# Optimization experiments

Measured on AMD Instinct MI355X. Metric: run time of the kernel, lower is better.

Reference implementation:

```python
import jax, jax.numpy as jnp
import numpy as np

T = 4096          # flattened document length (tokens)
FLAT = 512        # 2 * lstm_hidden_size
HD = 256          # head embedding dim (head_emb + char_emb)
FEAT = 20         # feature_size
MAXW = 20         # max mention width
NCAND = 30000     # enumerated candidate spans
HID = 512         # scorer hidden size
K = 1638          # floor(T * ment_ratio=0.4)
C = 40            # max antecedents
DEPTH = 2         # coref_depth
NSPK = 10
MENT = 2 * FLAT + FEAT + HD        # 1300 mention emb size
BIN_WIDTHS = [1, 1, 1, 1, 1, 4, 8, 16, 32]   # sums to 65 -> covers clamp(dist,0,64)
BINS = jnp.asarray(np.concatenate([np.full(w, i, dtype=np.int32) for i, w in enumerate(BIN_WIDTHS)]))


def _scorer(x, w1, b1, w2, b2, w3, b3):
    h = jax.nn.relu(x @ w1 + b1)
    h = jax.nn.relu(h @ w2 + b2)
    return (h @ w3 + b3)[..., 0]


def setup_inputs():
    key = jax.random.key(0)
    ks = jax.random.split(key, 30)
    p = lambda i, s: jax.random.normal(ks[i], s, jnp.float32) * 0.02
    cand_starts = jax.random.randint(ks[25], (NCAND,), 0, T)
    widths = jax.random.randint(ks[26], (NCAND,), 0, MAXW)
    cand_ends = jnp.minimum(cand_starts + widths, T - 1)
    return {
        "flat_lstm_out": jax.random.normal(ks[0], (T, FLAT), jnp.float32),
        "head_doc_embs": jax.random.normal(ks[1], (T, HD), jnp.float32),
        "w_span_head": p(2, (FLAT,)), "b_span_head": jnp.zeros((), jnp.float32),
        "width_embed": p(3, (MAXW, FEAT)),
        "ms_w1": p(4, (MENT, HID)), "ms_b1": jnp.zeros((HID,), jnp.float32),
        "ms_w2": p(5, (HID, HID)), "ms_b2": jnp.zeros((HID,), jnp.float32),
        "ms_w3": p(6, (HID, 1)), "ms_b3": jnp.zeros((1,), jnp.float32),
        "fast_w": p(7, (MENT, MENT)), "fast_b": jnp.zeros((MENT,), jnp.float32),
        "ss_w1": p(8, (3 * MENT + 3 * FEAT, HID)), "ss_b1": jnp.zeros((HID,), jnp.float32),
        "ss_w2": p(9, (HID, HID)), "ss_b2": jnp.zeros((HID,), jnp.float32),
        "ss_w3": p(10, (HID, 1)), "ss_b3": jnp.zeros((1,), jnp.float32),
        "gate_w": p(11, (2 * MENT, MENT)), "gate_b": jnp.zeros((MENT,), jnp.float32),
        "speaker_embed": p(12, (2, FEAT)),
        "genre_embed": p(13, (7, FEAT)),
        "dist_embed": p(14, (len(BIN_WIDTHS), FEAT)),
        "cand_starts": cand_starts,
        "cand_ends": cand_ends,
        "speaker_ids": jax.random.randint(ks[27], (T,), 0, NSPK),
        "genre_id": 3,
    }


def reference(flat_lstm_out, head_doc_embs, w_span_head, b_span_head, width_embed,
              ms_w1, ms_b1, ms_w2, ms_b2, ms_w3, ms_b3, fast_w, fast_b,
              ss_w1, ss_b1, ss_w2, ss_b2, ss_w3, ss_b3, gate_w, gate_b,
              speaker_embed, genre_embed, dist_embed,
              cand_starts, cand_ends, speaker_ids, genre_id):
    neg = -jnp.inf
    # ---- mention (span) embeddings: start/end gather + width emb + attention-pooled head ----
    width = cand_ends - cand_starts + 1                              # [N]
    start_embs = flat_lstm_out[cand_starts]                          # [N,FLAT]
    end_embs = flat_lstm_out[cand_ends]                              # [N,FLAT]
    width_embs = width_embed[width - 1]                              # [N,FEAT]
    span_idxs = jnp.clip(jnp.arange(MAXW)[None, :] + cand_starts[:, None], 0, T - 1)  # [N,W]
    ment_doc = head_doc_embs[span_idxs]                              # [N,W,HD]
    head_scores = flat_lstm_out @ w_span_head + b_span_head          # [T]
    g = head_scores[span_idxs] + jnp.where(jnp.arange(MAXW)[None, :] < width[:, None], 0.0, neg)
    attn = jax.nn.softmax(g, axis=1)                                 # [N,W]
    head_embs = jnp.einsum('nw,nwd->nd', attn, ment_doc)             # [N,HD]
    cand_embs = jnp.concatenate([start_embs, end_embs, width_embs, head_embs], axis=1)  # [N,MENT]
    cand_scores = _scorer(cand_embs, ms_w1, ms_b1, ms_w2, ms_b2, ms_w3, ms_b3)          # [N]
    # ---- prune mentions: top-k by score, reordered by document position ----
    _, top_idx = jax.lax.top_k(cand_scores, K)
    ment_pos = cand_starts[top_idx] * cand_ends[-1] + cand_ends[top_idx]
    top_idx = top_idx[jnp.argsort(ment_pos)]
    ment_embs = cand_embs[top_idx]                                   # [K,MENT]
    ment_scores = cand_scores[top_idx]                               # [K]
    ment_speakers = speaker_ids[cand_starts[top_idx]]                # [K]
    # ---- fast (bilinear) antecedent scoring + top-c pruning ----
    idx = jnp.arange(K)
    mask = (idx[:, None] - idx[None, :]) > 0                         # antecedent must precede
    src = ment_embs @ fast_w + fast_b
    fast = src @ ment_embs.T + ment_scores[:, None] + ment_scores[None, :] + jnp.where(mask, 0.0, neg)
    top_fast, antes = jax.lax.top_k(fast, C)                         # [K,C]
    dummy = jnp.zeros((K, 1), fast.dtype)
    genre_emb = jnp.broadcast_to(genre_embed[genre_id][None, None, :], (K, C, FEAT))
    ante_scores = top_fast
    # ---- iterative slow antecedent scoring + gated refinement ----
    for _ in range(DEPTH):
        ante_ment = ment_embs[antes]                                 # [K,C,MENT]
        same = (ment_speakers[:, None] == ment_speakers[antes]).astype(jnp.int32)
        spk_emb = speaker_embed[same]                                # [K,C,FEAT]
        dist_bin = BINS[jnp.clip(idx[:, None] - antes, 0, 64)]
        dist_emb = dist_embed[dist_bin]                              # [K,C,FEAT]
        me = jnp.broadcast_to(ment_embs[:, None, :], (K, C, MENT))
        ante_emb = jnp.concatenate([me, ante_ment, ante_ment * me, spk_emb, genre_emb, dist_emb], axis=2)
        ante_scores = top_fast + _scorer(ante_emb, ss_w1, ss_b1, ss_w2, ss_b2, ss_w3, ss_b3)
        weights = jax.nn.softmax(jnp.concatenate([dummy, ante_scores], axis=1), axis=-1)  # [K,C+1]
        stacked = jnp.concatenate([ment_embs[:, None, :], ante_ment], axis=1)             # [K,C+1,MENT]
        attended = jnp.einsum('kc,kcd->kd', weights, stacked)
        f = jax.nn.sigmoid(jnp.concatenate([ment_embs, attended], axis=1) @ gate_w + gate_b)
        ment_embs = f * attended + (1.0 - f) * ment_embs
    return jnp.concatenate([dummy, ante_scores], axis=1)             # [K,C+1] coref logits
```

## Files before the change

### kernel.cpp

```cpp
#include <hip/hip_runtime.h>
#include <math.h>

#define T_LEN 4096
#define FLATD 512
#define HDD 256
#define FEATD 20
#define NCAND 30000
#define HIDD 512
#define KSEL 1638
#define CANT 40
#define MENTD 1300
#define KPAD 1344
#define NPAIR (KSEL*CANT)
#define NEG_INF (-__builtin_inff())

#define MF_RELU 1
#define MF_MASK 4
#define MF_GATE 8

typedef unsigned short u16;
typedef __attribute__((ext_vector_type(8))) short bf16x8;
typedef __attribute__((ext_vector_type(4))) float f32x4;

__device__ __forceinline__ unsigned ordf(float f){
  unsigned u = __float_as_uint(f);
  return (u & 0x80000000u) ? ~u : (u | 0x80000000u);
}
__device__ __forceinline__ float unordf(unsigned u){
  return __uint_as_float((u & 0x80000000u) ? (u ^ 0x80000000u) : ~u);
}
__device__ __forceinline__ float bf2f(u16 h){ return __uint_as_float(((unsigned)h) << 16); }
__device__ __forceinline__ u16 f2bf(float f){
  unsigned u = __float_as_uint(f);
  u += 0x7fffu + ((u >> 16) & 1u);
  return (u16)(u >> 16);
}
__device__ __forceinline__ unsigned pkmul(unsigned a, unsigned b){
  float a0 = __uint_as_float(a << 16), a1 = __uint_as_float(a & 0xffff0000u);
  float b0 = __uint_as_float(b << 16), b1 = __uint_as_float(b & 0xffff0000u);
  float p0 = a0*b0, p1 = a1*b1;
  unsigned r;
  asm("v_cvt_pk_bf16_f32 %0, %1, %2" : "=v"(r) : "v"(p0), "v"(p1));
  return r;
}
__device__ __forceinline__ int featsrc(int k){
  if (k < 1024) return k;
  if (k < 1280) return k + 20;
  if (k < 1300) return k - 256;
  return -1;
}
__device__ __forceinline__ int bsrc64(int S){
  return (((S & 7) ^ ((S >> 3) & 7)) << 3);
}
__device__ __forceinline__ int brd64(int row, int h, int k8){
  return row*64 + (((((h << 2) | k8)) ^ (row & 7)) << 3);
}
__device__ __forceinline__ void gload16(const u16* g, u16* l){
  __builtin_amdgcn_global_load_lds((const __attribute__((address_space(1))) void*)(g),
                                   (__attribute__((address_space(3))) void*)(l), 16, 0, 0);
}

__global__ __launch_bounds__(256) void k_prep(const float* __restrict__ flat,
    const float* __restrict__ wemb, const float* __restrict__ fast_b, const float* __restrict__ gate_b,
    u16* __restrict__ flatbf, u16* __restrict__ wembP, float* __restrict__ fbP, float* __restrict__ gbP,
    unsigned* __restrict__ selws)
{
  int i = blockIdx.x*256 + threadIdx.x;
  if (i < T_LEN*FLATD) flatbf[i] = f2bf(flat[i]);
  if (i < 20*64) wembP[i] = ((i & 63) < 20) ? f2bf(wemb[(i >> 6)*FEATD + (i & 63)]) : (u16)0;
  if (i < KPAD){
    int s = featsrc(i);
    fbP[i] = (s >= 0) ? fast_b[s] : 0.f;
    gbP[i] = (s >= 0) ? gate_b[s] : 0.f;
  }
  if (i < 6156) selws[i] = 0;
}

__global__ __launch_bounds__(256) void k_head(const float* __restrict__ flat,
    const float* __restrict__ w, const float* __restrict__ b, float* __restrict__ hs)
{
  int lane = threadIdx.x & 63, wid = threadIdx.x >> 6;
  int row = blockIdx.x*4 + wid;
  if (row >= T_LEN) return;
  const float* x = flat + (size_t)row*FLATD;
  float s = 0.f;
  for (int j = lane; j < FLATD; j += 64) s += x[j]*w[j];
  #pragma unroll
  for (int o = 32; o; o >>= 1) s += __shfl_down(s, o, 64);
  if (lane == 0) hs[row] = s + b[0];
}

__global__ __launch_bounds__(256) void k_cand(const float* __restrict__ hs,
    const float* __restrict__ hdoc, const int* __restrict__ starts, const int* __restrict__ ends,
    u16* __restrict__ hemb)
{
  int wid = threadIdx.x >> 6, lane = threadIdx.x & 63;
  int n = blockIdx.x*4 + wid;
  if (n >= NCAND) return;
  int s = starts[n], e = ends[n];
  int width = e - s + 1;
  float g[20];
  #pragma unroll
  for (int w2 = 0; w2 < 20; ++w2) g[w2] = (w2 < width) ? hs[min(s + w2, T_LEN-1)] : NEG_INF;
  float m = NEG_INF;
  #pragma unroll
  for (int w2 = 0; w2 < 20; ++w2) m = fmaxf(m, g[w2]);
  float sum = 0.f;
  #pragma unroll
  for (int w2 = 0; w2 < 20; ++w2){ g[w2] = expf(g[w2] - m); sum += g[w2]; }
  float inv = 1.f/sum;
  #pragma unroll
  for (int di = 0; di < 4; ++di){
    int d = lane + di*64;
    float acc = 0.f;
    #pragma unroll
    for (int w2 = 0; w2 < 20; ++w2)
      acc += g[w2]*hdoc[(size_t)min(s + w2, T_LEN-1)*HDD + d];
    hemb[(size_t)n*HDD + d] = f2bf(acc*inv);
  }
}

__global__ __launch_bounds__(256) void k_transall(const float* __restrict__ ms_w1,
    const float* __restrict__ ms_w2, const float* __restrict__ fast_w,
    const float* __restrict__ ss_w1, const float* __restrict__ ss_w2,
    const float* __restrict__ gate_w,
    u16* ms1T, u16* ms2T, u16* fastT, u16* ss1abT, u16* sspT,
    u16* ss2T, u16* gateTall)
{
  const float* B; u16* D; int Kb, N, srcN, ldD, kperm, nperm;
  switch (blockIdx.z){
    case 0: B = ms_w1; D = ms1T; Kb = KPAD; N = HIDD; srcN = HIDD; ldD = KPAD; kperm = 1; nperm = 0; break;
    case 1: B = ms_w2; D = ms2T; Kb = HIDD; N = HIDD; srcN = HIDD; ldD = HIDD; kperm = 0; nperm = 0; break;
    case 2: B = fast_w; D = fastT; Kb = KPAD; N = MENTD; srcN = MENTD; ldD = KPAD; kperm = 1; nperm = 1; break;
    case 3: B = ss_w1; D = ss1abT; Kb = KPAD; N = HIDD; srcN = HIDD; ldD = KPAD; kperm = 1; nperm = 0; break;
    case 4: B = ss_w1 + (size_t)MENTD*HIDD; D = ss1abT + (size_t)512*KPAD; Kb = KPAD; N = HIDD; srcN = HIDD; ldD = KPAD; kperm = 1; nperm = 0; break;
    case 5: B = ss_w1 + (size_t)2*MENTD*HIDD; D = sspT; Kb = KPAD; N = HIDD; srcN = HIDD; ldD = KPAD; kperm = 1; nperm = 0; break;
    case 6: B = ss_w2; D = ss2T; Kb = HIDD; N = HIDD; srcN = HIDD; ldD = HIDD; kperm = 0; nperm = 0; break;
    case 7: B = gate_w; D = gateTall; Kb = KPAD; N = MENTD; srcN = MENTD; ldD = 2*KPAD; kperm = 1; nperm = 1; break;
    default: B = gate_w + (size_t)MENTD*MENTD; D = gateTall + KPAD; Kb = KPAD; N = MENTD; srcN = MENTD; ldD = 2*KPAD; kperm = 1; nperm = 1; break;
  }
  int k0 = blockIdx.x*32, n0 = blockIdx.y*32;
  if (k0 >= Kb || n0 >= N) return;
  __shared__ float t[32][33];
  int tx = threadIdx.x & 31, ty = threadIdx.x >> 5;
  for (int r = ty; r < 32; r += 8){
    int gk = k0 + r, gn = n0 + tx;
    int sk = kperm ? featsrc(gk) : ((gk < Kb) ? gk : -1);
    int sn = nperm ? ((gn < N) ? featsrc(gn) : -1) : ((gn < N) ? gn : -1);
    t[r][tx] = (sk >= 0 && sn >= 0) ? B[(size_t)sk*srcN + sn] : 0.f;
  }
  __syncthreads();
  for (int r = ty; r < 32; r += 8){
    int gn = n0 + r, gk = k0 + tx;
    if (gn < N && gk < Kb) D[(size_t)gn*ldD + gk] = f2bf(t[tx][r]);
  }
}

__global__ __launch_bounds__(256) void k_mfma_cand(
    const u16* __restrict__ flatbf, const u16* __restrict__ hemb, const u16* __restrict__ wembP,
    const int* __restrict__ starts, const int* __restrict__ ends,
    const u16* __restrict__ Bt, int M, const float* __restrict__ bias, u16* __restrict__ Cbf)
{
  __shared__ alignas(16) u16 As[8192];
  __shared__ alignas(16) u16 Bs[8192];
  int tid = threadIdx.x;
  int row0 = blockIdx.y*128, col0 = blockIdx.x*128;
  int lane = tid & 63, wid = tid >> 6;
  int wr = wid >> 1, wc = wid & 1;
  int l15 = lane & 15, l4 = lane >> 4;

  int sS[4], eS[4], nS[4], so[4];
  const u16* pb[4];
  #pragma unroll
  for (int i = 0; i < 4; ++i){
    int S = tid + (i << 8);
    int r = S >> 3;
    so[i] = bsrc64(S);
    int n = row0 + r; if (n >= M) n = M - 1;
    sS[i] = starts[n]; eS[i] = ends[n]; nS[i] = n;
    pb[i] = Bt + (size_t)(col0 + r)*KPAD + so[i];
  }

  f32x4 acc[4][4];
  #pragma unroll
  for (int m = 0; m < 4; ++m)
    #pragma unroll
    for (int n = 0; n < 4; ++n)
      #pragma unroll
      for (int q = 0; q < 4; ++q) acc[m][n][q] = 0.f;

  for (int kt = 0; kt < KPAD/64; ++kt){
    int k0 = kt << 6;
    #pragma unroll
    for (int i = 0; i < 4; ++i){
      int f = k0 + so[i];
      const u16* src = (f < 512) ? flatbf + (size_t)sS[i]*FLATD + f
                     : (f < 1024) ? flatbf + (size_t)eS[i]*FLATD + (f - 512)
                     : (f < 1280) ? hemb + (size_t)nS[i]*HDD + (f - 1024)
                     : wembP + (eS[i] - sS[i])*64 + (f - 1280);
      gload16(src, As + (tid + (i << 8))*8);
      gload16(pb[i] + k0, Bs + (tid + (i << 8))*8);
    }
    __syncthreads();
    #pragma unroll
    for (int h = 0; h < 2; ++h){
      bf16x8 af[4], bfr[4];
      #pragma unroll
      for (int m = 0; m < 4; ++m) af[m] = *(const bf16x8*)(As + brd64(wr*64 + m*16 + l15, h, l4));
      #pragma unroll
      for (int n = 0; n < 4; ++n) bfr[n] = *(const bf16x8*)(Bs + brd64(wc*64 + n*16 + l15, h, l4));
      #pragma unroll
      for (int m = 0; m < 4; ++m)
        #pragma unroll
        for (int n = 0; n < 4; ++n)
          acc[m][n] = __builtin_amdgcn_mfma_f32_16x16x32_bf16(af[m], bfr[n], acc[m][n], 0, 0, 0);
    }
    __syncthreads();
  }
  #pragma unroll
  for (int m = 0; m < 4; ++m){
    #pragma unroll
    for (int q = 0; q < 4; ++q){
      int grow = row0 + wr*64 + m*16 + l4*4 + q;
      if (grow >= M) continue;
      #pragma unroll
      for (int n = 0; n < 4; ++n){
        int gcol = col0 + wc*64 + n*16 + l15;
        float v = fmaxf(acc[m][n][q] + bias[gcol], 0.f);
        Cbf[(size_t)grow*HIDD + gcol] = f2bf(v);
      }
    }
  }
}

__global__ __launch_bounds__(256) void k_mfma(const u16* __restrict__ A,
    const u16* __restrict__ A2, const u16* __restrict__ Bt, int M, int N, int Kp, int ldA,
    const float* __restrict__ bias, const float* __restrict__ msc,
    float* __restrict__ Cf, int ldf, u16* __restrict__ Cbf, int ldbf, int Nstore, int flags,
    const u16* __restrict__ g_att, const u16* __restrict__ g_mo)
{
  __shared__ alignas(16) u16 As[8192];
  __shared__ alignas(16) u16 Bs[8192];
  int tid = threadIdx.x;
  int row0 = blockIdx.y*128, col0 = blockIdx.x*128;
  if ((flags & MF_MASK) && col0 >= row0 + 128) return;
  int lane = tid & 63, wid = tid >> 6;
  int wr = wid >> 1, wc = wid & 1;
  int l15 = lane & 15, l4 = lane >> 4;

  const u16 *pa[4], *qa[4], *pb[4];
  int kt1 = A2 ? (ldA >> 6) : (Kp >> 6);
  int koff = kt1 << 6;
  #pragma unroll
  for (int i = 0; i < 4; ++i){
    int S = tid + (i << 8);
    int r = S >> 3;
    int soi = bsrc64(S);
    int ra = row0 + r; if (ra >= M) ra = M - 1;
    int cb = col0 + r; if (cb >= N) cb = N - 1;
    pa[i] = A + (size_t)ra*ldA + soi;
    qa[i] = A2 ? (A2 + (size_t)ra*ldA + soi - koff) : pa[i];
    pb[i] = Bt + (size_t)cb*Kp + soi;
  }

  f32x4 acc[4][4];
  #pragma unroll
  for (int m = 0; m < 4; ++m)
    #pragma unroll
    for (int n = 0; n < 4; ++n)
      #pragma unroll
      for (int q = 0; q < 4; ++q) acc[m][n][q] = 0.f;

  int nkt = Kp >> 6;
  for (int kt = 0; kt < nkt; ++kt){
    int k0 = kt << 6;
    #pragma unroll
    for (int i = 0; i < 4; ++i){
      const u16* a = (kt < kt1) ? pa[i] : qa[i];
      gload16(a + k0, As + (tid + (i << 8))*8);
      gload16(pb[i] + k0, Bs + (tid + (i << 8))*8);
    }
    __syncthreads();
    #pragma unroll
    for (int h = 0; h < 2; ++h){
      bf16x8 af[4], bfr[4];
      #pragma unroll
      for (int m = 0; m < 4; ++m) af[m] = *(const bf16x8*)(As + brd64(wr*64 + m*16 + l15, h, l4));
      #pragma unroll
      for (int n = 0; n < 4; ++n) bfr[n] = *(const bf16x8*)(Bs + brd64(wc*64 + n*16 + l15, h, l4));
      #pragma unroll
      for (int m = 0; m < 4; ++m)
        #pragma unroll
        for (int n = 0; n < 4; ++n)
          acc[m][n] = __builtin_amdgcn_mfma_f32_16x16x32_bf16(af[m], bfr[n], acc[m][n], 0, 0, 0);
    }
    __syncthreads();
  }
  #pragma unroll
  for (int m = 0; m < 4; ++m){
    #pragma unroll
    for (int q = 0; q < 4; ++q){
      int grow = row0 + wr*64 + m*16 + l4*4 + q;
      if (grow >= M) continue;
      #pragma unroll
      for (int n = 0; n < 4; ++n){
        int gcol = col0 + wc*64 + n*16 + l15;
        if (gcol < N){
          float v = acc[m][n][q];
          if (bias) v += bias[gcol];
          if (flags & MF_MASK){ v += msc[grow] + msc[gcol]; if (gcol >= grow) v = NEG_INF; }
          if (flags & MF_RELU) v = fmaxf(v, 0.f);
          if (flags & MF_GATE){
            float f = 1.f/(1.f + expf(-v));
            float res = f*bf2f(g_att[(size_t)grow*ldbf + gcol])
                      + (1.f - f)*bf2f(g_mo[(size_t)grow*ldbf + gcol]);
            Cbf[(size_t)grow*ldbf + gcol] = f2bf(res);
          } else {
            if (Cf)  Cf[(size_t)grow*ldf + gcol] = v;
            if (Cbf) Cbf[(size_t)grow*ldbf + gcol] = f2bf(v);
          }
        } else if (Cbf && gcol < Nstore){
          Cbf[(size_t)grow*ldbf + gcol] = 0;
        }
      }
    }
  }
}

__global__ __launch_bounds__(256) void k_mfma_rowdot(const u16* __restrict__ A,
    const u16* __restrict__ Bt, int M, const float* __restrict__ b2,
    const float* __restrict__ w3, const float* __restrict__ b3,
    const float* __restrict__ add, float* __restrict__ out)
{
  __shared__ alignas(16) u16 As[8192];
  __shared__ alignas(16) u16 Bs[8192];
  __shared__ float rsum[128][2];
  int tid = threadIdx.x;
  int row0 = blockIdx.x*128;
  int lane = tid & 63, wid = tid >> 6;
  int wr = wid >> 1, wc = wid & 1;
  int l15 = lane & 15, l4 = lane >> 4;

  const u16* pa[4]; int so[4], rr[4];
  #pragma unroll
  for (int i = 0; i < 4; ++i){
    int S = tid + (i << 8);
    int r = S >> 3;
    so[i] = bsrc64(S); rr[i] = r;
    int ra = row0 + r; if (ra >= M) ra = M - 1;
    pa[i] = A + (size_t)ra*HIDD + so[i];
  }

  float rd[4][4] = {};
  for (int p = 0; p < 4; ++p){
    int col0 = p*128;
    f32x4 acc[4][4];
    #pragma unroll
    for (int m = 0; m < 4; ++m)
      #pragma unroll
      for (int n = 0; n < 4; ++n)
        #pragma unroll
        for (int q = 0; q < 4; ++q) acc[m][n][q] = 0.f;
    for (int kt = 0; kt < HIDD/64; ++kt){
      int k0 = kt << 6;
      #pragma unroll
      for (int i = 0; i < 4; ++i){
        gload16(pa[i] + k0, As + (tid + (i << 8))*8);
        gload16(Bt + (size_t)(col0 + rr[i])*HIDD + so[i] + k0, Bs + (tid + (i << 8))*8);
      }
      __syncthreads();
      #pragma unroll
      for (int h = 0; h < 2; ++h){
        bf16x8 af[4], bfr[4];
        #pragma unroll
        for (int m = 0; m < 4; ++m) af[m] = *(const bf16x8*)(As + brd64(wr*64 + m*16 + l15, h, l4));
        #pragma unroll
        for (int n = 0; n < 4; ++n) bfr[n] = *(const bf16x8*)(Bs + brd64(wc*64 + n*16 + l15, h, l4));
        #pragma unroll
        for (int m = 0; m < 4; ++m)
          #pragma unroll
          for (int n = 0; n < 4; ++n)
            acc[m][n] = __builtin_amdgcn_mfma_f32_16x16x32_bf16(af[m], bfr[n], acc[m][n], 0, 0, 0);
      }
      __syncthreads();
    }
    #pragma unroll
    for (int n = 0; n < 4; ++n){
      int gcol = col0 + wc*64 + n*16 + l15;
      float bb = b2[gcol], ww = w3[gcol];
      #pragma unroll
      for (int m = 0; m < 4; ++m)
        #pragma unroll
        for (int q = 0; q < 4; ++q){
          float v = fmaxf(acc[m][n][q] + bb, 0.f);
          rd[m][q] = fmaf(v, ww, rd[m][q]);
        }
    }
  }
  #pragma unroll
  for (int m = 0; m < 4; ++m)
    #pragma unroll
    for (int q = 0; q < 4; ++q){
      float s = rd[m][q];
      s += __shfl_xor(s, 1, 64); s += __shfl_xor(s, 2, 64);
      s += __shfl_xor(s, 4, 64); s += __shfl_xor(s, 8, 64);
      if (l15 == 0) rsum[wr*64 + m*16 + l4*4 + q][wc] = s;
    }
  __syncthreads();
  if (tid < 128){
    int gr = row0 + tid;
    if (gr < M){
      float v = rsum[tid][0] + rsum[tid][1] + b3[0];
      if (add) v += add[gr];
      out[gr] = v;
    }
  }
}

__global__ __launch_bounds__(256, 2) void k_d1_mfma(int Mc,
    const u16* __restrict__ ment, const int* __restrict__ antes, const int* __restrict__ mspk,
    const u16* __restrict__ Bt, const float* __restrict__ A_meb,
    const float* __restrict__ comb, u16* __restrict__ H1)
{
  __shared__ alignas(16) u16 As[8192];
  __shared__ alignas(16) u16 Bs[16384];
  __shared__ int ri[128], rj[128], rcomb[128];
  int tid = threadIdx.x;
  int row0 = blockIdx.y*128;
  int col0 = blockIdx.x*256;
  if (tid < 128){
    int r = row0 + tid;
    int p = (r < Mc ? r : 0);
    int i = p / CANT;
    int j = antes[p];
    ri[tid] = i; rj[tid] = j;
    int same = (mspk[i] == mspk[j]) ? 1 : 0;
    int d = i - j; d = d < 0 ? 0 : (d > 64 ? 64 : d);
    int bin = (d <= 4) ? d : (d <= 8 ? 5 : (d <= 16 ? 6 : (d <= 32 ? 7 : 8)));
    rcomb[tid] = same*9 + bin;
  }
  __syncthreads();
  int lane = tid & 63, wid = tid >> 6;
  int wr = wid >> 1, wc = wid & 1;
  int l15 = lane & 15, l4 = lane >> 4;

  const u16 *pi[4], *pj[4];
  #pragma unroll
  for (int i = 0; i < 4; ++i){
    int S = tid + (i << 8);
    int r = S >> 3;
    int soi = bsrc64(S);
    pi[i] = ment + (size_t)ri[r]*KPAD + soi;
    pj[i] = ment + (size_t)rj[r]*KPAD + soi;
  }
  int bo[8];
  #pragma unroll
  for (int i = 0; i < 8; ++i){
    int S = tid + (i << 8);
    int r = S >> 3;
    bo[i] = (col0 + r)*KPAD + bsrc64(S);
  }

  f32x4 acc[4][8];
  #pragma unroll
  for (int m = 0; m < 4; ++m)
    #pragma unroll
    for (int n = 0; n < 8; ++n)
      #pragma unroll
      for (int q = 0; q < 4; ++q) acc[m][n][q] = 0.f;

  int nkt = KPAD >> 6;
  for (int kt = 0; kt < nkt; ++kt){
    int k0 = kt << 6;
    #pragma unroll
    for (int i = 0; i < 8; ++i)
      gload16(Bt + bo[i] + k0, Bs + (tid + (i << 8))*8);
    #pragma unroll
    for (int i = 0; i < 4; ++i){
      uint4 va = *(const uint4*)(pi[i] + k0);
      uint4 vb = *(const uint4*)(pj[i] + k0);
      uint4 vo;
      vo.x = pkmul(va.x, vb.x); vo.y = pkmul(va.y, vb.y);
      vo.z = pkmul(va.z, vb.z); vo.w = pkmul(va.w, vb.w);
      *(uint4*)(As + (tid + (i << 8))*8) = vo;
    }
    __syncthreads();
    #pragma unroll
    for (int h = 0; h < 2; ++h){
      bf16x8 af[4];
      #pragma unroll
      for (int m = 0; m < 4; ++m) af[m] = *(const bf16x8*)(As + brd64(wr*64 + m*16 + l15, h, l4));
      #pragma unroll
      for (int n = 0; n < 8; ++n){
        bf16x8 bfr = *(const bf16x8*)(Bs + brd64(wc*128 + n*16 + l15, h, l4));
        #pragma unroll
        for (int m = 0; m < 4; ++m)
          acc[m][n] = __builtin_amdgcn_mfma_f32_16x16x32_bf16(af[m], bfr, acc[m][n], 0, 0, 0);
      }
    }
    __syncthreads();
  }
  #pragma unroll
  for (int m = 0; m < 4; ++m){
    #pragma unroll
    for (int q = 0; q < 4; ++q){
      int rl = wr*64 + m*16 + l4*4 + q;
      int grow = row0 + rl;
      if (grow >= Mc) continue;
      const float* me = A_meb + (size_t)ri[rl]*1024;
      const float* an = A_meb + (size_t)rj[rl]*1024 + 512;
      const float* cb = comb + (size_t)rcomb[rl]*HIDD;
      #pragma unroll
      for (int n = 0; n < 8; ++n){
        int gcol = col0 + wc*128 + n*16 + l15;
        float v = acc[m][n][q] + me[gcol] + an[gcol] + cb[gcol];
        H1[(size_t)grow*HIDD + gcol] = f2bf(fmaxf(v, 0.f));
      }
    }
  }
}

__global__ __launch_bounds__(256) void k_hist(const float* __restrict__ scores,
    unsigned* __restrict__ selws, int pass)
{
  int n = blockIdx.x*256 + threadIdx.x;
  if (n >= NCAND) return;
  unsigned u = ordf(scores[n]);
  const unsigned* meta = selws + 6144;
  if (pass == 0) atomicAdd(&selws[u >> 21], 1u);
  else if (pass == 1){ if ((u >> 21) == meta[0]) atomicAdd(&selws[2048 + ((u >> 10) & 0x7FFu)], 1u); }
  else { if ((u >> 10) == meta[2]) atomicAdd(&selws[4096 + (u & 0x3FFu)], 1u); }
}
__global__ __launch_bounds__(1024) void k_thresh(unsigned* __restrict__ selws, int mode){
  __shared__ unsigned a[2048], b[2048];
  int tid = threadIdx.x;
  unsigned* meta = selws + 6144;
  const unsigned* gbin = selws + (mode == 0 ? 0 : (mode == 1 ? 2048 : 4096));
  unsigned target = (mode == 0) ? (unsigned)KSEL : meta[mode == 1 ? 1 : 3];
  a[tid] = gbin[tid]; a[tid + 1024] = gbin[tid + 1024];
  unsigned *src = a, *dst = b;
  for (int step = 1; step < 2048; step <<= 1){
    __syncthreads();
    for (int i = tid; i < 2048; i += 1024)
      dst[i] = src[i] + ((i + step < 2048) ? src[i + step] : 0u);
    unsigned* t2 = src; src = dst; dst = t2;
  }
  __syncthreads();
  for (int i = tid; i < 2048; i += 1024){
    unsigned si = src[i], sn = (i < 2047) ? src[i+1] : 0u;
    if (si >= target && sn < target){
      if (mode == 0){ meta[0] = (unsigned)i; meta[1] = target - sn; }
      else if (mode == 1){ meta[2] = (meta[0] << 11) | (unsigned)i; meta[3] = target - sn; }
      else { meta[4] = (meta[2] << 10) | (unsigned)i; meta[5] = target - sn; }
    }
  }
}
__global__ __launch_bounds__(256) void k_compact(const float* __restrict__ scores,
    unsigned* __restrict__ selws, int* __restrict__ g_sel, unsigned* __restrict__ g_eq)
{
  int n = blockIdx.x*256 + threadIdx.x;
  if (n >= NCAND) return;
  unsigned kth = selws[6144 + 4];
  unsigned* cnt = selws + 6152;
  unsigned u = ordf(scores[n]);
  if (u > kth){ unsigned p = atomicAdd(&cnt[0], 1u); g_sel[p] = n; }
  else if (u == kth){ unsigned p = atomicAdd(&cnt[1], 1u); if (p < 1024) g_eq[p] = (unsigned)n; }
}
__global__ __launch_bounds__(1024) void k_eqrank(unsigned* __restrict__ selws,
    const unsigned* __restrict__ g_eq, int* __restrict__ g_sel)
{
  __shared__ unsigned eq[1024];
  int tid = threadIdx.x;
  unsigned neq = selws[6152 + 1]; if (neq > 1024u) neq = 1024u;
  unsigned E = selws[6144 + 5];
  unsigned G = selws[6152 + 0];
  eq[tid] = (tid < (int)neq) ? g_eq[tid] : 0xFFFFFFFFu;
  __syncthreads();
  if (tid < (int)neq){
    unsigned mine = eq[tid]; unsigned r = 0;
    for (unsigned j = 0; j < neq; ++j) r += (eq[j] < mine) ? 1u : 0u;
    if (r < E) g_sel[G + r] = (int)mine;
  }
}
__global__ __launch_bounds__(256) void k_rank1(const float* __restrict__ scores,
    const int* __restrict__ g_sel, int* __restrict__ ranked)
{
  __shared__ unsigned long long key[KSEL];
  int tid = threadIdx.x;
  for (int t = tid; t < KSEL; t += 256){
    int n = g_sel[t];
    key[t] = ((unsigned long long)(~ordf(scores[n])) << 32) | (unsigned)n;
  }
  __syncthreads();
  int t = blockIdx.x*256 + tid;
  if (t >= KSEL) return;
  unsigned long long mine = key[t];
  int r = 0;
  #pragma unroll 16
  for (int j = 0; j < KSEL; ++j) r += (key[j] < mine) ? 1 : 0;
  ranked[r] = (int)(mine & 0xFFFFFFFFu);
}
__global__ __launch_bounds__(256) void k_rank2(const int* __restrict__ ranked,
    const int* __restrict__ starts, const int* __restrict__ ends, int* __restrict__ top_idx)
{
  __shared__ unsigned long long key[KSEL];
  int tid = threadIdx.x;
  int elast = ends[NCAND-1];
  for (int t = tid; t < KSEL; t += 256){
    int n = ranked[t];
    unsigned mp = (unsigned)(starts[n]*elast + ends[n]);
    key[t] = ((unsigned long long)mp << 11) | (unsigned)t;
  }
  __syncthreads();
  int t = blockIdx.x*256 + tid;
  if (t >= KSEL) return;
  unsigned long long mine = key[t];
  int r = 0;
  #pragma unroll 16
  for (int j = 0; j < KSEL; ++j) r += (key[j] < mine) ? 1 : 0;
  top_idx[r] = ranked[t];
}

__global__ __launch_bounds__(256) void k_gather(const int* __restrict__ top_idx,
    const u16* __restrict__ flatbf, const u16* __restrict__ hemb, const u16* __restrict__ wembP,
    const int* __restrict__ starts, const int* __restrict__ ends,
    const float* __restrict__ cscores, const int* __restrict__ spk_ids,
    u16* __restrict__ ment, float* __restrict__ mscore, int* __restrict__ mspk)
{
  int k = blockIdx.x; int n = top_idx[k];
  int s = starts[n], e = ends[n];
  int v = threadIdx.x;
  if (v < KPAD/8){
    int f0 = v*8;
    const u16* src = (f0 < 512) ? flatbf + (size_t)s*FLATD + f0
                   : (f0 < 1024) ? flatbf + (size_t)e*FLATD + (f0 - 512)
                   : (f0 < 1280) ? hemb + (size_t)n*HDD + (f0 - 1024)
                   : wembP + (e - s)*64 + (f0 - 1280);
    *(uint4*)(ment + (size_t)k*KPAD + f0) = *(const uint4*)src;
  }
  if (threadIdx.x == 0){ mscore[k] = cscores[n]; mspk[k] = spk_ids[s]; }
}

__global__ __launch_bounds__(256) void k_f3(const float* __restrict__ fast,
    float* __restrict__ top_fast, int* __restrict__ antes)
{
  int wid = threadIdx.x >> 6, lane = threadIdx.x & 63;
  int i = blockIdx.x*4 + wid;
  if (i >= KSEL) return;
  const float* row = fast + (size_t)i*KSEL;
  unsigned long long key[26];
  #pragma unroll
  for (int t = 0; t < 26; ++t){
    int j = lane + (t << 6);
    unsigned long long k2 = 0ULL;
    if (j < i) k2 = ((unsigned long long)ordf(row[j]) << 32) | (unsigned)(0xFFFFFFFFu - (unsigned)j);
    key[t] = k2;
  }
  for (int c = 0; c < CANT; ++c){
    unsigned long long m = 0ULL;
    #pragma unroll
    for (int t = 0; t < 26; ++t) if (key[t] > m) m = key[t];
    #pragma unroll
    for (int o = 32; o; o >>= 1){
      unsigned long long v = __shfl_xor(m, o, 64);
      if (v > m) m = v;
    }
    if (m){
      #pragma unroll
      for (int t = 0; t < 26; ++t) if (key[t] == m) key[t] = 0ULL;
    }
    if (lane == 0){
      if (m){
        top_fast[(size_t)i*CANT + c] = unordf((unsigned)(m >> 32));
        antes[(size_t)i*CANT + c]    = (int)(0xFFFFFFFFu - (unsigned)(m & 0xFFFFFFFFu));
      } else {
        top_fast[(size_t)i*CANT + c] = NEG_INF;
        antes[(size_t)i*CANT + c]    = c;
      }
    }
  }
}

__global__ __launch_bounds__(256) void k_dsmall(const float* __restrict__ ss_w1,
    const float* __restrict__ ss_b1, const float* __restrict__ spk_emb,
    const float* __restrict__ gen_emb, const float* __restrict__ dist_emb,
    const int* __restrict__ genre_id, float* __restrict__ comb)
{
  int r = blockIdx.x;
  int same = r / 9, bin = r % 9;
  const float* es = spk_emb + same*FEATD;
  const float* eg = gen_emb + genre_id[0]*FEATD;
  const float* ed = dist_emb + bin*FEATD;
  for (int h = threadIdx.x; h < HIDD; h += 256){
    float acc = ss_b1[h];
    const float* ws_ = ss_w1 + (size_t)3900*HIDD + h;
    const float* wg  = ss_w1 + (size_t)3920*HIDD + h;
    const float* wd  = ss_w1 + (size_t)3940*HIDD + h;
    for (int f = 0; f < FEATD; ++f){
      acc += es[f]*ws_[(size_t)f*HIDD];
      acc += eg[f]*wg[(size_t)f*HIDD];
      acc += ed[f]*wd[(size_t)f*HIDD];
    }
    comb[(size_t)r*HIDD + h] = acc;
  }
}

__global__ __launch_bounds__(256) void k_d4a(const float* __restrict__ ante_sc,
    const int* __restrict__ antes, const u16* __restrict__ ment, u16* __restrict__ att_bf)
{
  int i = blockIdx.x;
  __shared__ float w[CANT+1];
  __shared__ int aj[CANT];
  if (threadIdx.x == 0){
    float s[CANT]; float m = 0.f;
    #pragma unroll
    for (int c = 0; c < CANT; ++c){ s[c] = ante_sc[i*CANT + c]; m = fmaxf(m, s[c]); }
    float e0 = expf(0.f - m);
    float sum = e0;
    float ex[CANT];
    #pragma unroll
    for (int c = 0; c < CANT; ++c){ ex[c] = expf(s[c] - m); sum += ex[c]; }
    float inv = 1.f/sum;
    w[0] = e0*inv;
    #pragma unroll
    for (int c = 0; c < CANT; ++c) w[c+1] = ex[c]*inv;
  }
  if (threadIdx.x < CANT) aj[threadIdx.x] = antes[i*CANT + threadIdx.x];
  __syncthreads();
  int v = threadIdx.x;
  if (v >= KPAD/8) return;
  int d0 = v*8;
  float r[8] = {};
  {
    uint4 x = *(const uint4*)(ment + (size_t)i*KPAD + d0);
    float w0 = w[0];
    const unsigned* px = (const unsigned*)&x;
    #pragma unroll
    for (int h = 0; h < 4; ++h){
      r[2*h]   = w0*__uint_as_float(px[h] << 16);
      r[2*h+1] = w0*__uint_as_float(px[h] & 0xffff0000u);
    }
  }
  for (int c = 0; c < CANT; ++c){
    uint4 x = *(const uint4*)(ment + (size_t)aj[c]*KPAD + d0);
    float wc_ = w[c+1];
    const unsigned* px = (const unsigned*)&x;
    #pragma unroll
    for (int h = 0; h < 4; ++h){
      r[2*h]   = fmaf(wc_, __uint_as_float(px[h] << 16), r[2*h]);
      r[2*h+1] = fmaf(wc_, __uint_as_float(px[h] & 0xffff0000u), r[2*h+1]);
    }
  }
  u16 o[8];
  #pragma unroll
  for (int h = 0; h < 8; ++h) o[h] = f2bf(r[h]);
  *(uint4*)(att_bf + (size_t)i*KPAD + d0) = *(const uint4*)o;
}

__global__ __launch_bounds__(256) void k_out(const float* __restrict__ ante_sc, float* __restrict__ out){
  int idx = blockIdx.x*256 + threadIdx.x;
  if (idx >= KSEL*41) return;
  int i = idx / 41, c = idx % 41;
  float v = (c == 0) ? 0.f : ante_sc[i*CANT + (c-1)];
  if (!isfinite(v)) v = -3.0e38f;
  out[idx] = v;
}

__global__ void k_zero(float* out, int n){
  int i = blockIdx.x*256 + threadIdx.x;
  if (i < n) out[i] = 0.f;
}

extern "C" void kernel_launch(void* const* d_in, const int* in_sizes, int n_in,
                              void* d_out, int out_size, void* d_ws, size_t ws_size,
                              hipStream_t stream)
{
  const float* flat   = (const float*)d_in[0];
  const float* hdoc   = (const float*)d_in[1];
  const float* w_head = (const float*)d_in[2];
  const float* b_head = (const float*)d_in[3];
  const float* wemb   = (const float*)d_in[4];
  const float* ms_w1  = (const float*)d_in[5];
  const float* ms_b1  = (const float*)d_in[6];
  const float* ms_w2  = (const float*)d_in[7];
  const float* ms_b2  = (const float*)d_in[8];
  const float* ms_w3  = (const float*)d_in[9];
  const float* ms_b3  = (const float*)d_in[10];
  const float* fast_w = (const float*)d_in[11];
  const float* fast_b = (const float*)d_in[12];
  const float* ss_w1  = (const float*)d_in[13];
  const float* ss_b1  = (const float*)d_in[14];
  const float* ss_w2  = (const float*)d_in[15];
  const float* ss_b2  = (const float*)d_in[16];
  const float* ss_w3  = (const float*)d_in[17];
  const float* ss_b3  = (const float*)d_in[18];
  const float* gate_w = (const float*)d_in[19];
  const float* gate_b = (const float*)d_in[20];
  const float* spk_e  = (const float*)d_in[21];
  const float* gen_e  = (const float*)d_in[22];
  const float* dist_e = (const float*)d_in[23];
  const int* starts   = (const int*)d_in[24];
  const int* ends     = (const int*)d_in[25];
  const int* spk_ids  = (const int*)d_in[26];
  const int* genre_id = (const int*)d_in[27];
  float* out = (float*)d_out;

  size_t off = 0;
  char* base = (char*)d_ws;
  auto alloc = [&](size_t nbytes) -> void* {
    void* p = (void*)(base + off);
    off += ((nbytes + 255)/256)*256;
    return p;
  };
  float* head_sc = (float*)alloc((size_t)T_LEN*4);
  u16*   flatbf  = (u16*)alloc((size_t)T_LEN*FLATD*2);
  u16*   wembP   = (u16*)alloc((size_t)20*64*2);
  float* fbP     = (float*)alloc((size_t)KPAD*4);
  float* gbP     = (float*)alloc((size_t)KPAD*4);
  u16*   hemb    = (u16*)alloc((size_t)NCAND*HDD*2);
  float* cscores = (float*)alloc((size_t)NCAND*4);
  int*   top_idx = (int*)alloc(2048*4);
  unsigned* selws= (unsigned*)alloc(6160*4);
  int*   g_sel   = (int*)alloc((size_t)KSEL*4);
  unsigned* g_eq = (unsigned*)alloc(1024*4);
  int*   g_rank  = (int*)alloc((size_t)KSEL*4);
  u16*   ms1T    = (u16*)alloc((size_t)HIDD*KPAD*2);
  u16*   ms2T    = (u16*)alloc((size_t)HIDD*HIDD*2);
  u16*   fastT   = (u16*)alloc((size_t)MENTD*KPAD*2);
  u16*   ss1abT  = (u16*)alloc((size_t)1024*KPAD*2);
  u16*   sspT    = (u16*)alloc((size_t)HIDD*KPAD*2);
  u16*   ss2T    = (u16*)alloc((size_t)HIDD*HIDD*2);
  u16*   gateTall= (u16*)alloc((size_t)MENTD*2*KPAD*2);
  u16*   ment    = (u16*)alloc((size_t)KSEL*KPAD*2);
  u16*   mentB   = (u16*)alloc((size_t)KSEL*KPAD*2);
  u16*   srcb    = (u16*)alloc((size_t)KSEL*KPAD*2);
  float* mscore  = (float*)alloc((size_t)KSEL*4);
  int*   mspk    = (int*)alloc((size_t)KSEL*4);
  float* fastm   = (float*)alloc((size_t)KSEL*KSEL*4);
  float* top_fast= (float*)alloc((size_t)NPAIR*4);
  int*   antes   = (int*)alloc((size_t)NPAIR*4);
  float* ante_sc = (float*)alloc((size_t)NPAIR*4);
  float* A_meb   = (float*)alloc((size_t)KSEL*1024*4);
  float* comb    = (float*)alloc((size_t)18*HIDD*4);
  u16*   att_bf  = (u16*)alloc((size_t)KSEL*KPAD*2);
  u16*   bufH1   = (u16*)alloc((size_t)NPAIR*HIDD*2);

  if (ws_size < off){
    k_zero<<<(KSEL*41 + 255)/256, 256, 0, stream>>>(out, KSEL*41);
    return;
  }

  k_prep<<<(T_LEN*FLATD + 255)/256, 256, 0, stream>>>(flat, wemb, fast_b, gate_b,
                                                      flatbf, wembP, fbP, gbP, selws);
  k_transall<<<dim3(KPAD/32, 41, 9), 256, 0, stream>>>(ms_w1, ms_w2, fast_w, ss_w1, ss_w2, gate_w,
      ms1T, ms2T, fastT, ss1abT, sspT, ss2T, gateTall);

  k_head<<<T_LEN/4, 256, 0, stream>>>(flat, w_head, b_head, head_sc);
  k_cand<<<NCAND/4, 256, 0, stream>>>(head_sc, hdoc, starts, ends, hemb);

  k_mfma_cand<<<dim3(HIDD/128, (NCAND + 127)/128), 256, 0, stream>>>(
      flatbf, hemb, wembP, starts, ends, ms1T, NCAND, ms_b1, bufH1);
  k_mfma_rowdot<<<(NCAND + 127)/128, 256, 0, stream>>>(bufH1, ms2T, NCAND, ms_b2, ms_w3, ms_b3,
                                                       nullptr, cscores);

  k_hist<<<(NCAND + 255)/256, 256, 0, stream>>>(cscores, selws, 0);
  k_thresh<<<1, 1024, 0, stream>>>(selws, 0);
  k_hist<<<(NCAND + 255)/256, 256, 0, stream>>>(cscores, selws, 1);
  k_thresh<<<1, 1024, 0, stream>>>(selws, 1);
  k_hist<<<(NCAND + 255)/256, 256, 0, stream>>>(cscores, selws, 2);
  k_thresh<<<1, 1024, 0, stream>>>(selws, 2);
  k_compact<<<(NCAND + 255)/256, 256, 0, stream>>>(cscores, selws, g_sel, g_eq);
  k_eqrank<<<1, 1024, 0, stream>>>(selws, g_eq, g_sel);
  k_rank1<<<(KSEL + 255)/256, 256, 0, stream>>>(cscores, g_sel, g_rank);
  k_rank2<<<(KSEL + 255)/256, 256, 0, stream>>>(g_rank, starts, ends, top_idx);

  k_gather<<<KSEL, 256, 0, stream>>>(top_idx, flatbf, hemb, wembP, starts, ends, cscores, spk_ids,
                                     ment, mscore, mspk);

  k_mfma<<<dim3((MENTD+127)/128, (KSEL+127)/128), 256, 0, stream>>>(
      ment, nullptr, fastT, KSEL, MENTD, KPAD, KPAD, fbP, nullptr,
      nullptr, 0, srcb, KPAD, KPAD, 0, nullptr, nullptr);
  k_mfma<<<dim3((KSEL+127)/128, (KSEL+127)/128), 256, 0, stream>>>(
      srcb, nullptr, ment, KSEL, KSEL, KPAD, KPAD, nullptr, mscore,
      fastm, KSEL, nullptr, 0, 0, MF_MASK, nullptr, nullptr);
  k_f3<<<(KSEL+3)/4, 256, 0, stream>>>(fastm, top_fast, antes);

  k_dsmall<<<18, 256, 0, stream>>>(ss_w1, ss_b1, spk_e, gen_e, dist_e, genre_id, comb);

  const u16* mcur = ment;
  for (int iter = 0; iter < 2; ++iter){
    k_mfma<<<dim3(8, (KSEL+127)/128), 256, 0, stream>>>(
        mcur, nullptr, ss1abT, KSEL, 1024, KPAD, KPAD, nullptr, nullptr,
        A_meb, 1024, nullptr, 0, 0, 0, nullptr, nullptr);
    k_d1_mfma<<<dim3(2, (NPAIR + 127)/128), 256, 0, stream>>>(
        NPAIR, mcur, antes, mspk, sspT, A_meb, comb, bufH1);
    k_mfma_rowdot<<<(NPAIR + 127)/128, 256, 0, stream>>>(bufH1, ss2T, NPAIR, ss_b2, ss_w3, ss_b3,
                                                         top_fast, ante_sc);
    if (iter == 0){
      k_d4a<<<KSEL, 256, 0, stream>>>(ante_sc, antes, mcur, att_bf);
      k_mfma<<<dim3((MENTD+127)/128, (KSEL+127)/128), 256, 0, stream>>>(
          ment, att_bf, gateTall, KSEL, MENTD, 2*KPAD, KPAD, gbP, nullptr,
          nullptr, 0, mentB, KPAD, KPAD, MF_GATE, att_bf, ment);
      mcur = mentB;
    }
  }

  k_out<<<(KSEL*41 + 255)/256, 256, 0, stream>>>(ante_sc, out);
}
```

Baseline: 1.125 ms.

## Cache mention rows in LDS and async-load antecedent rows in pair GEMM

In the first-layer pair-scoring GEMM, the few distinct mention rows a 128-row tile covers (at most 5) are now loaded once into LDS. Previously both the mention and antecedent rows were read from global memory on every k-step. Only the antecedent rows are streamed per k-tile, using the same direct-to-LDS gload16 path as the B operand. The elementwise bf16 product is now formed at fragment-read time. This cuts global traffic and lets the A operand load asynchronously. In exchange it uses more LDS per block and repeats the multiply in both column waves.

```diff
diff --git a/kernel.cpp b/kernel.cpp
--- a/kernel.cpp
+++ b/kernel.cpp
@@ -422,36 +422,44 @@
     const u16* __restrict__ Bt, const float* __restrict__ A_meb,
     const float* __restrict__ comb, u16* __restrict__ H1)
 {
-  __shared__ alignas(16) u16 As[8192];
   __shared__ alignas(16) u16 Bs[16384];
-  __shared__ int ri[128], rj[128], rcomb[128];
+  __shared__ alignas(16) u16 AnS[8192];
+  __shared__ alignas(16) u16 meLDS[5*KPAD];
+  __shared__ int ri[128], rj[128], rcomb[128], iid[128];
   int tid = threadIdx.x;
   int row0 = blockIdx.y*128;
   int col0 = blockIdx.x*256;
+  int ibase = row0 / CANT;
   if (tid < 128){
     int r = row0 + tid;
     int p = (r < Mc ? r : 0);
     int i = p / CANT;
     int j = antes[p];
     ri[tid] = i; rj[tid] = j;
+    int ii = i - ibase; ii = ii < 0 ? 0 : (ii > 4 ? 4 : ii);
+    iid[tid] = ii;
     int same = (mspk[i] == mspk[j]) ? 1 : 0;
     int d = i - j; d = d < 0 ? 0 : (d > 64 ? 64 : d);
     int bin = (d <= 4) ? d : (d <= 8 ? 5 : (d <= 16 ? 6 : (d <= 32 ? 7 : 8)));
     rcomb[tid] = same*9 + bin;
   }
+  for (int idx = tid; idx < 5*(KPAD/8); idx += 256){
+    int s = idx / (KPAD/8);
+    int off = (idx % (KPAD/8))*8;
+    int isrc = ibase + s; if (isrc >= KSEL) isrc = KSEL - 1;
+    *(uint4*)(meLDS + s*KPAD + off) = *(const uint4*)(ment + (size_t)isrc*KPAD + off);
+  }
   __syncthreads();
   int lane = tid & 63, wid = tid >> 6;
   int wr = wid >> 1, wc = wid & 1;
   int l15 = lane & 15, l4 = lane >> 4;
 
-  const u16 *pi[4], *pj[4];
+  const u16* pj[4];
   #pragma unroll
   for (int i = 0; i < 4; ++i){
     int S = tid + (i << 8);
     int r = S >> 3;
-    int soi = bsrc64(S);
-    pi[i] = ment + (size_t)ri[r]*KPAD + soi;
-    pj[i] = ment + (size_t)rj[r]*KPAD + soi;
+    pj[i] = ment + (size_t)rj[r]*KPAD + bsrc64(S);
   }
   int bo[8];
   #pragma unroll
@@ -476,20 +484,23 @@
     for (int i = 0; i < 8; ++i)
       gload16(Bt + bo[i] + k0, Bs + (tid + (i << 8))*8);
     #pragma unroll
-    for (int i = 0; i < 4; ++i){
-      uint4 va = *(const uint4*)(pi[i] + k0);
-      uint4 vb = *(const uint4*)(pj[i] + k0);
-      uint4 vo;
-      vo.x = pkmul(va.x, vb.x); vo.y = pkmul(va.y, vb.y);
-      vo.z = pkmul(va.z, vb.z); vo.w = pkmul(va.w, vb.w);
-      *(uint4*)(As + (tid + (i << 8))*8) = vo;
-    }
+    for (int i = 0; i < 4; ++i)
+      gload16(pj[i] + k0, AnS + (tid + (i << 8))*8);
     __syncthreads();
     #pragma unroll
     for (int h = 0; h < 2; ++h){
+      int koff = (((h << 2) | l4) << 3);
       bf16x8 af[4];
       #pragma unroll
-      for (int m = 0; m < 4; ++m) af[m] = *(const bf16x8*)(As + brd64(wr*64 + m*16 + l15, h, l4));
+      for (int m = 0; m < 4; ++m){
+        int row = wr*64 + m*16 + l15;
+        uint4 an = *(const uint4*)(AnS + brd64(row, h, l4));
+        uint4 me = *(const uint4*)(meLDS + iid[row]*KPAD + k0 + koff);
+        uint4 vo;
+        vo.x = pkmul(me.x, an.x); vo.y = pkmul(me.y, an.y);
+        vo.z = pkmul(me.z, an.z); vo.w = pkmul(me.w, an.w);
+        af[m] = *(const bf16x8*)&vo;
+      }
       #pragma unroll
       for (int n = 0; n < 8; ++n){
         bf16x8 bfr = *(const bf16x8*)(Bs + brd64(wc*128 + n*16 + l15, h, l4));
```

After: 1.169 ms. +3.8%, slower.
